# Kernel tuning notes

Hardware: AMD Instinct MI355X
Metric: run time of the kernel (lower is better)

The kernel has to match this reference:

```python
import jax, jax.numpy as jnp
import numpy as np

N_NODES = 200000
N_BONDS = 220000
D = 128


def setup_inputs() -> dict:
    key = jax.random.key(0)
    ks = jax.random.split(key, 8)
    h = jax.random.normal(ks[0], (N_NODES, D), dtype=jnp.float32)
    src = jax.random.randint(ks[1], (N_BONDS,), 0, N_NODES, dtype=jnp.int64)
    dst = jax.random.randint(ks[2], (N_BONDS,), 0, N_NODES, dtype=jnp.int64)
    # MLP params (Sequential: Linear(256,128)+ReLU, Linear(128,128)+ReLU, Linear(128,2))
    W1 = jax.random.normal(ks[3], (2 * D, 128), dtype=jnp.float32) * (1.0 / np.sqrt(2 * D))
    b1 = jnp.zeros((128,), dtype=jnp.float32)
    W2 = jax.random.normal(ks[4], (128, 128), dtype=jnp.float32) * (1.0 / np.sqrt(128))
    b2 = jnp.zeros((128,), dtype=jnp.float32)
    W3 = jax.random.normal(ks[5], (128, 2), dtype=jnp.float32) * (1.0 / np.sqrt(128))
    b3 = jnp.zeros((2,), dtype=jnp.float32)
    return {"h": h, "src": src, "dst": dst,
            "W1": W1, "b1": b1, "W2": W2, "b2": b2, "W3": W3, "b3": b3}


def _mlp(x, W1, b1, W2, b2, W3, b3):
    x = jax.nn.relu(x @ W1 + b1)
    x = jax.nn.relu(x @ W2 + b2)
    return x @ W3 + b3


def reference(h, src, dst, W1, b1, W2, b2, W3, b3):
    # forward edges: (src -> dst); reverse edges: (dst -> src)
    h_src = h[src]            # [E, D] gather
    h_dst = h[dst]            # [E, D] gather
    h_forward = jnp.concatenate([h_src, h_dst], axis=1)  # [E, 2D]
    h_reverse = jnp.concatenate([h_dst, h_src], axis=1)  # [E, 2D]
    return (_mlp(h_forward, W1, b1, W2, b2, W3, b3)
            + _mlp(h_reverse, W1, b1, W2, b2, W3, b3))
```

## Files before the change

kernel.cpp:

```cpp
#include <hip/hip_runtime.h>
#include <hip/hip_bf16.h>
#include <stdint.h>


typedef __attribute__((ext_vector_type(8))) short bf16x8;
typedef __attribute__((ext_vector_type(4))) float f32x4;

__device__ __forceinline__ float bf2f(unsigned u16) {
    union { unsigned u; float f; } v; v.u = u16 << 16;
    return v.f;
}
__device__ __forceinline__ unsigned short f2bf(float f) {
    union { float f; unsigned u; } v; v.f = f;
    unsigned u = v.u;
    unsigned r = u + 0x7FFFu + ((u >> 16) & 1u);
    return (unsigned short)(r >> 16);
}

__device__ __forceinline__ int swz(int f, int c) {
    return f * 128 + ((c ^ (f & 7)) << 3);
}

__device__ __forceinline__ bf16x8 cvt8(const float* p) {
    float4 x = *(const float4*)p;
    float4 y = *(const float4*)(p + 4);
    union { bf16x8 v; __hip_bfloat162 h[4]; } R;
    R.h[0] = __float22bfloat162_rn(float2{x.x, x.y});
    R.h[1] = __float22bfloat162_rn(float2{x.z, x.w});
    R.h[2] = __float22bfloat162_rn(float2{y.x, y.y});
    R.h[3] = __float22bfloat162_rn(float2{y.z, y.w});
    return R.v;
}

__device__ __forceinline__ bf16x8 addrelu8(uint4 a, uint4 b) {
    union { uint4 v; unsigned u[4]; } A, B;
    A.v = a; B.v = b;
    union { bf16x8 v; __hip_bfloat162 h[4]; } R;
#pragma unroll
    for (int i = 0; i < 4; ++i) {
        float a0 = bf2f(A.u[i] & 0xFFFFu), a1 = bf2f(A.u[i] >> 16);
        float b0 = bf2f(B.u[i] & 0xFFFFu), b1 = bf2f(B.u[i] >> 16);
        R.h[i] = __float22bfloat162_rn(float2{fmaxf(a0 + b0, 0.f),
                                              fmaxf(a1 + b1, 0.f)});
    }
    return R.v;
}

#define MFMA(a, b, c) __builtin_amdgcn_mfma_f32_16x16x32_bf16((a), (b), (c), 0, 0, 0)

__global__ void prep_weights(const float* __restrict__ W1,
                             const float* __restrict__ W2,
                             unsigned short* __restrict__ W1t,
                             unsigned short* __restrict__ W2t) {
    int idx = blockIdx.x * 256 + threadIdx.x;
    if (idx < 256 * 128) {
        int j = idx >> 7, k = idx & 127;
        float v = (j < 128) ? W1[k * 128 + j] : W1[(k + 128) * 128 + (j - 128)];
        W1t[idx] = f2bf(v);
    } else {
        int i2 = idx - 256 * 128;
        if (i2 < 128 * 128) {
            int n = i2 >> 7, k = i2 & 127;
            W2t[i2] = f2bf(W2[k * 128 + n]);
        }
    }
}

__global__ __launch_bounds__(512, 2) void node_proj(
    const float* __restrict__ h, const unsigned short* __restrict__ W1t,
    const float* __restrict__ b1, unsigned short* __restrict__ P, int nodes) {
    __shared__ unsigned short W1s[256 * 128];

    int t = threadIdx.x;
    int lane = t & 63;
    int wv = t >> 6;
    int ml = lane & 15, quad = lane >> 4;

    {
        int r = t >> 1, half = t & 1;
        const uint4* src = (const uint4*)(W1t + (size_t)r * 128 + half * 64);
#pragma unroll
        for (int i = 0; i < 8; ++i)
            *(uint4*)(W1s + swz(r, half * 8 + i)) = src[i];
    }

    int node = blockIdx.x * 128 + wv * 16 + ml;
    int nodeL = (node < nodes) ? node : (nodes - 1);
    const float* hrow = h + (size_t)nodeL * 128;
    bf16x8 bfrag[4];
#pragma unroll
    for (int kk = 0; kk < 4; ++kk)
        bfrag[kk] = cvt8(hrow + kk * 32 + quad * 8);

    __syncthreads();

    f32x4 acc[16] = {};
#pragma unroll
    for (int kk = 0; kk < 4; ++kk) {
#pragma unroll
        for (int ct = 0; ct < 16; ++ct) {
            bf16x8 afrag = *(const bf16x8*)(W1s + swz(ct * 16 + ml, kk * 4 + quad));
            acc[ct] = MFMA(afrag, bfrag[kk], acc[ct]);
        }
    }

    if (node < nodes) {
        unsigned short* prow = P + (size_t)node * 256;
#pragma unroll
        for (int ct = 0; ct < 16; ++ct) {
            int fbase = ct * 16 + quad * 4;
            float v0 = acc[ct][0], v1 = acc[ct][1];
            float v2 = acc[ct][2], v3 = acc[ct][3];
            if (fbase >= 128) {
                float4 bv = *(const float4*)(b1 + (fbase - 128));
                v0 += bv.x; v1 += bv.y; v2 += bv.z; v3 += bv.w;
            }
            union { uint2 u; __hip_bfloat162 h2[2]; } o;
            o.h2[0] = __float22bfloat162_rn(float2{v0, v1});
            o.h2[1] = __float22bfloat162_rn(float2{v2, v3});
            *(uint2*)(prow + fbase) = o.u;
        }
    }
}

__global__ __launch_bounds__(512, 2) void edge_mlp(
    const unsigned short* __restrict__ P, const int* __restrict__ src,
    const int* __restrict__ dst, const unsigned short* __restrict__ W2t,
    const float* __restrict__ b2, const float* __restrict__ W3,
    const float* __restrict__ b3, float* __restrict__ out, int E) {
    __shared__ unsigned short W2s[128 * 128];

    int t = threadIdx.x;
    int lane = t & 63;
    int wv = t >> 6;
    int ml = lane & 15, quad = lane >> 4;

    {
        int f = t >> 2, q4 = t & 3;
        const uint4* s = (const uint4*)(W2t + (size_t)f * 128 + q4 * 32);
#pragma unroll
        for (int i = 0; i < 4; ++i)
            *(uint4*)(W2s + swz(f, q4 * 4 + i)) = s[i];
    }

    int e = blockIdx.x * 128 + wv * 16 + ml;
    int ec = (e < E) ? e : (E - 1);
    int si = src[ec], di = dst[ec];
    const unsigned short* Ps = P + (size_t)si * 256;
    const unsigned short* Pd = P + (size_t)di * 256;

    uint4 g[4][4];
#pragma unroll
    for (int kk = 0; kk < 4; ++kk) {
        int ko = kk * 32 + quad * 8;
        g[kk][0] = *(const uint4*)(Ps + ko);
        g[kk][1] = *(const uint4*)(Ps + 128 + ko);
        g[kk][2] = *(const uint4*)(Pd + ko);
        g[kk][3] = *(const uint4*)(Pd + 128 + ko);
    }

    __syncthreads();

    f32x4 acc[2][8] = {};
#pragma unroll
    for (int kk = 0; kk < 4; ++kk) {
        bf16x8 afw = addrelu8(g[kk][0], g[kk][3]);
        bf16x8 arv = addrelu8(g[kk][2], g[kk][1]);
#pragma unroll
        for (int ct = 0; ct < 8; ++ct) {
            bf16x8 bfrag = *(const bf16x8*)(W2s + swz(ct * 16 + ml, kk * 4 + quad));
            acc[0][ct] = MFMA(afw, bfrag, acc[0][ct]);
            acc[1][ct] = MFMA(arv, bfrag, acc[1][ct]);
        }
    }

    float w30[8], w31[8], b2v[8];
#pragma unroll
    for (int ct = 0; ct < 8; ++ct) {
        int c = ct * 16 + ml;
        w30[ct] = W3[c * 2 + 0];
        w31[ct] = W3[c * 2 + 1];
        b2v[ct] = b2[c];
    }
    float p0[2][4], p1[2][4];
#pragma unroll
    for (int rt = 0; rt < 2; ++rt)
#pragma unroll
        for (int reg = 0; reg < 4; ++reg) { p0[rt][reg] = 0.f; p1[rt][reg] = 0.f; }
#pragma unroll
    for (int rt = 0; rt < 2; ++rt)
#pragma unroll
        for (int ct = 0; ct < 8; ++ct)
#pragma unroll
            for (int reg = 0; reg < 4; ++reg) {
                float h2 = fmaxf(acc[rt][ct][reg] + b2v[ct], 0.f);
                p0[rt][reg] += h2 * w30[ct];
                p1[rt][reg] += h2 * w31[ct];
            }
#pragma unroll
    for (int m = 1; m < 16; m <<= 1) {
#pragma unroll
        for (int rt = 0; rt < 2; ++rt)
#pragma unroll
            for (int reg = 0; reg < 4; ++reg) {
                p0[rt][reg] += __shfl_xor(p0[rt][reg], m);
                p1[rt][reg] += __shfl_xor(p1[rt][reg], m);
            }
    }

    if (ml < 2) {
        float bb = 2.f * b3[ml];
#pragma unroll
        for (int reg = 0; reg < 4; ++reg) {
            int ee = blockIdx.x * 128 + wv * 16 + quad * 4 + reg;
            if (ee < E) {
                float v = (ml == 0) ? (p0[0][reg] + p0[1][reg])
                                    : (p1[0][reg] + p1[1][reg]);
                out[(size_t)ee * 2 + ml] = v + bb;
            }
        }
    }
}

extern "C" void kernel_launch(void* const* d_in, const int* in_sizes, int n_in,
                              void* d_out, int out_size, void* d_ws, size_t ws_size,
                              hipStream_t stream) {
    (void)n_in; (void)out_size; (void)ws_size;
    const float* h  = (const float*)d_in[0];
    const int*   sr = (const int*)d_in[1];
    const int*   ds = (const int*)d_in[2];
    const float* W1 = (const float*)d_in[3];
    const float* b1 = (const float*)d_in[4];
    const float* W2 = (const float*)d_in[5];
    const float* b2 = (const float*)d_in[6];
    const float* W3 = (const float*)d_in[7];
    const float* b3 = (const float*)d_in[8];
    float* out = (float*)d_out;

    int nodes = in_sizes[0] / 128;
    int E = in_sizes[1];

    unsigned short* W1t = (unsigned short*)d_ws;
    unsigned short* W2t = W1t + 256 * 128;
    unsigned short* P   = W2t + 128 * 128;

    prep_weights<<<(256 * 128 + 128 * 128 + 255) / 256, 256, 0, stream>>>(W1, W2, W1t, W2t);

    int ntiles = (nodes + 127) / 128;
    node_proj<<<ntiles, 512, 0, stream>>>(h, W1t, b1, P, nodes);

    int etiles = (E + 127) / 128;
    edge_mlp<<<etiles, 512, 0, stream>>>(P, sr, ds, W2t, b2, W3, b3, out, E);
}
```

Measured before the change: 245.8 us.

## Make node_proj and edge_mlp persistent with software-prefetched next-tile loads

Both kernels become grid-stride persistent loops (node_proj capped at 512 blocks, edge_mlp at 256). The weight matrix is staged into LDS once per block instead of once per tile. While the current tile runs its MFMAs, the next tile's h rows or gathered P rows are loaded into registers, and the edge kernel also fetches edge indices two tiles ahead. This targets repeated weight-staging cost and exposed gather latency, at the price of extra register pressure and fewer resident blocks for latency hiding.

```diff
diff --git a/kernel.cpp b/kernel.cpp
--- a/kernel.cpp
+++ b/kernel.cpp
@@ -21,9 +21,7 @@
     return f * 128 + ((c ^ (f & 7)) << 3);
 }
 
-__device__ __forceinline__ bf16x8 cvt8(const float* p) {
-    float4 x = *(const float4*)p;
-    float4 y = *(const float4*)(p + 4);
+__device__ __forceinline__ bf16x8 cvt8r(float4 x, float4 y) {
     union { bf16x8 v; __hip_bfloat162 h[4]; } R;
     R.h[0] = __float22bfloat162_rn(float2{x.x, x.y});
     R.h[1] = __float22bfloat162_rn(float2{x.z, x.w});
@@ -68,7 +66,8 @@
 
 __global__ __launch_bounds__(512, 2) void node_proj(
     const float* __restrict__ h, const unsigned short* __restrict__ W1t,
-    const float* __restrict__ b1, unsigned short* __restrict__ P, int nodes) {
+    const float* __restrict__ b1, unsigned short* __restrict__ P,
+    int nodes, int ntiles) {
     __shared__ unsigned short W1s[256 * 128];
 
     int t = threadIdx.x;
@@ -84,41 +83,67 @@
             *(uint4*)(W1s + swz(r, half * 8 + i)) = src[i];
     }
 
-    int node = blockIdx.x * 128 + wv * 16 + ml;
-    int nodeL = (node < nodes) ? node : (nodes - 1);
-    const float* hrow = h + (size_t)nodeL * 128;
-    bf16x8 bfrag[4];
-#pragma unroll
-    for (int kk = 0; kk < 4; ++kk)
-        bfrag[kk] = cvt8(hrow + kk * 32 + quad * 8);
+    int tile = blockIdx.x;
+    float4 hreg[8];
+    if (tile < ntiles) {
+        int nd = tile * 128 + wv * 16 + ml;
+        if (nd >= nodes) nd = nodes - 1;
+        const float4* hp = (const float4*)(h + (size_t)nd * 128);
+#pragma unroll
+        for (int kk = 0; kk < 4; ++kk) {
+            hreg[2 * kk]     = hp[kk * 8 + quad * 2];
+            hreg[2 * kk + 1] = hp[kk * 8 + quad * 2 + 1];
+        }
+    }
 
     __syncthreads();
 
-    f32x4 acc[16] = {};
-#pragma unroll
-    for (int kk = 0; kk < 4; ++kk) {
-#pragma unroll
-        for (int ct = 0; ct < 16; ++ct) {
-            bf16x8 afrag = *(const bf16x8*)(W1s + swz(ct * 16 + ml, kk * 4 + quad));
-            acc[ct] = MFMA(afrag, bfrag[kk], acc[ct]);
-        }
-    }
-
-    if (node < nodes) {
-        unsigned short* prow = P + (size_t)node * 256;
-#pragma unroll
-        for (int ct = 0; ct < 16; ++ct) {
-            int fbase = ct * 16 + quad * 4;
-            float v0 = acc[ct][0], v1 = acc[ct][1];
-            float v2 = acc[ct][2], v3 = acc[ct][3];
-            if (fbase >= 128) {
-                float4 bv = *(const float4*)(b1 + (fbase - 128));
-                v0 += bv.x; v1 += bv.y; v2 += bv.z; v3 += bv.w;
-            }
-            union { uint2 u; __hip_bfloat162 h2[2]; } o;
-            o.h2[0] = __float22bfloat162_rn(float2{v0, v1});
-            o.h2[1] = __float22bfloat162_rn(float2{v2, v3});
-            *(uint2*)(prow + fbase) = o.u;
+    for (; tile < ntiles; tile += gridDim.x) {
+        bf16x8 bfrag[4];
+#pragma unroll
+        for (int kk = 0; kk < 4; ++kk)
+            bfrag[kk] = cvt8r(hreg[2 * kk], hreg[2 * kk + 1]);
+
+        int node = tile * 128 + wv * 16 + ml;
+
+        int ntile = tile + gridDim.x;
+        if (ntile < ntiles) {
+            int nd = ntile * 128 + wv * 16 + ml;
+            if (nd >= nodes) nd = nodes - 1;
+            const float4* hp = (const float4*)(h + (size_t)nd * 128);
+#pragma unroll
+            for (int kk = 0; kk < 4; ++kk) {
+                hreg[2 * kk]     = hp[kk * 8 + quad * 2];
+                hreg[2 * kk + 1] = hp[kk * 8 + quad * 2 + 1];
+            }
+        }
+
+        f32x4 acc[16] = {};
+#pragma unroll
+        for (int kk = 0; kk < 4; ++kk) {
+#pragma unroll
+            for (int ct = 0; ct < 16; ++ct) {
+                bf16x8 afrag = *(const bf16x8*)(W1s + swz(ct * 16 + ml, kk * 4 + quad));
+                acc[ct] = MFMA(afrag, bfrag[kk], acc[ct]);
+            }
+        }
+
+        if (node < nodes) {
+            unsigned short* prow = P + (size_t)node * 256;
+#pragma unroll
+            for (int ct = 0; ct < 16; ++ct) {
+                int fbase = ct * 16 + quad * 4;
+                float v0 = acc[ct][0], v1 = acc[ct][1];
+                float v2 = acc[ct][2], v3 = acc[ct][3];
+                if (fbase >= 128) {
+                    float4 bv = *(const float4*)(b1 + (fbase - 128));
+                    v0 += bv.x; v1 += bv.y; v2 += bv.z; v3 += bv.w;
+                }
+                union { uint2 u; __hip_bfloat162 h2[2]; } o;
+                o.h2[0] = __float22bfloat162_rn(float2{v0, v1});
+                o.h2[1] = __float22bfloat162_rn(float2{v2, v3});
+                *(uint2*)(prow + fbase) = o.u;
+            }
         }
     }
 }
@@ -127,7 +152,7 @@
     const unsigned short* __restrict__ P, const int* __restrict__ src,
     const int* __restrict__ dst, const unsigned short* __restrict__ W2t,
     const float* __restrict__ b2, const float* __restrict__ W3,
-    const float* __restrict__ b3, float* __restrict__ out, int E) {
+    const float* __restrict__ b3, float* __restrict__ out, int E, int etiles) {
     __shared__ unsigned short W2s[128 * 128];
 
     int t = threadIdx.x;
@@ -141,37 +166,6 @@
 #pragma unroll
         for (int i = 0; i < 4; ++i)
             *(uint4*)(W2s + swz(f, q4 * 4 + i)) = s[i];
-    }
-
-    int e = blockIdx.x * 128 + wv * 16 + ml;
-    int ec = (e < E) ? e : (E - 1);
-    int si = src[ec], di = dst[ec];
-    const unsigned short* Ps = P + (size_t)si * 256;
-    const unsigned short* Pd = P + (size_t)di * 256;
-
-    uint4 g[4][4];
-#pragma unroll
-    for (int kk = 0; kk < 4; ++kk) {
-        int ko = kk * 32 + quad * 8;
-        g[kk][0] = *(const uint4*)(Ps + ko);
-        g[kk][1] = *(const uint4*)(Ps + 128 + ko);
-        g[kk][2] = *(const uint4*)(Pd + ko);
-        g[kk][3] = *(const uint4*)(Pd + 128 + ko);
-    }
-
-    __syncthreads();
-
-    f32x4 acc[2][8] = {};
-#pragma unroll
-    for (int kk = 0; kk < 4; ++kk) {
-        bf16x8 afw = addrelu8(g[kk][0], g[kk][3]);
-        bf16x8 arv = addrelu8(g[kk][2], g[kk][1]);
-#pragma unroll
-        for (int ct = 0; ct < 8; ++ct) {
-            bf16x8 bfrag = *(const bf16x8*)(W2s + swz(ct * 16 + ml, kk * 4 + quad));
-            acc[0][ct] = MFMA(afw, bfrag, acc[0][ct]);
-            acc[1][ct] = MFMA(arv, bfrag, acc[1][ct]);
-        }
     }
 
     float w30[8], w31[8], b2v[8];
@@ -182,41 +176,112 @@
         w31[ct] = W3[c * 2 + 1];
         b2v[ct] = b2[c];
     }
-    float p0[2][4], p1[2][4];
-#pragma unroll
-    for (int rt = 0; rt < 2; ++rt)
-#pragma unroll
-        for (int reg = 0; reg < 4; ++reg) { p0[rt][reg] = 0.f; p1[rt][reg] = 0.f; }
-#pragma unroll
-    for (int rt = 0; rt < 2; ++rt)
-#pragma unroll
-        for (int ct = 0; ct < 8; ++ct)
+    float bb0 = 2.f * b3[0], bb1 = 2.f * b3[1];
+
+    int tile = blockIdx.x;
+
+    int si = 0, di = 0, si2 = 0, di2 = 0;
+    uint4 g[4][4];
+    if (tile < etiles) {
+        int e0 = tile * 128 + wv * 16 + ml;
+        int ec = (e0 < E) ? e0 : (E - 1);
+        si = src[ec]; di = dst[ec];
+        const unsigned short* Ps = P + (size_t)si * 256;
+        const unsigned short* Pd = P + (size_t)di * 256;
+#pragma unroll
+        for (int kk = 0; kk < 4; ++kk) {
+            int ko = kk * 32 + quad * 8;
+            g[kk][0] = *(const uint4*)(Ps + ko);
+            g[kk][1] = *(const uint4*)(Ps + 128 + ko);
+            g[kk][2] = *(const uint4*)(Pd + ko);
+            g[kk][3] = *(const uint4*)(Pd + 128 + ko);
+        }
+        int t2 = tile + gridDim.x;
+        if (t2 < etiles) {
+            int e2 = t2 * 128 + wv * 16 + ml;
+            int ec2 = (e2 < E) ? e2 : (E - 1);
+            si2 = src[ec2]; di2 = dst[ec2];
+        }
+    }
+
+    __syncthreads();
+
+    for (; tile < etiles; tile += gridDim.x) {
+        bf16x8 afw[4], arv[4];
+#pragma unroll
+        for (int kk = 0; kk < 4; ++kk) {
+            afw[kk] = addrelu8(g[kk][0], g[kk][3]);
+            arv[kk] = addrelu8(g[kk][2], g[kk][1]);
+        }
+
+        int ebase = tile * 128 + wv * 16;
+
+        int ntile = tile + gridDim.x;
+        if (ntile < etiles) {
+            const unsigned short* Ps = P + (size_t)si2 * 256;
+            const unsigned short* Pd = P + (size_t)di2 * 256;
+#pragma unroll
+            for (int kk = 0; kk < 4; ++kk) {
+                int ko = kk * 32 + quad * 8;
+                g[kk][0] = *(const uint4*)(Ps + ko);
+                g[kk][1] = *(const uint4*)(Ps + 128 + ko);
+                g[kk][2] = *(const uint4*)(Pd + ko);
+                g[kk][3] = *(const uint4*)(Pd + 128 + ko);
+            }
+            int t2 = ntile + gridDim.x;
+            if (t2 < etiles) {
+                int e2 = t2 * 128 + wv * 16 + ml;
+                int ec2 = (e2 < E) ? e2 : (E - 1);
+                si2 = src[ec2]; di2 = dst[ec2];
+            }
+        }
+
+        f32x4 acc[2][8] = {};
+#pragma unroll
+        for (int kk = 0; kk < 4; ++kk) {
+#pragma unroll
+            for (int ct = 0; ct < 8; ++ct) {
+                bf16x8 bfrag = *(const bf16x8*)(W2s + swz(ct * 16 + ml, kk * 4 + quad));
+                acc[0][ct] = MFMA(afw[kk], bfrag, acc[0][ct]);
+                acc[1][ct] = MFMA(arv[kk], bfrag, acc[1][ct]);
+            }
+        }
+
+        float p0[2][4], p1[2][4];
+#pragma unroll
+        for (int rt = 0; rt < 2; ++rt)
+#pragma unroll
+            for (int reg = 0; reg < 4; ++reg) { p0[rt][reg] = 0.f; p1[rt][reg] = 0.f; }
+#pragma unroll
+        for (int rt = 0; rt < 2; ++rt)
+#pragma unroll
+            for (int ct = 0; ct < 8; ++ct)
+#pragma unroll
+                for (int reg = 0; reg < 4; ++reg) {
+                    float h2 = fmaxf(acc[rt][ct][reg] + b2v[ct], 0.f);
+                    p0[rt][reg] += h2 * w30[ct];
+                    p1[rt][reg] += h2 * w31[ct];
+                }
+#pragma unroll
+        for (int m = 1; m < 16; m <<= 1) {
+#pragma unroll
+            for (int rt = 0; rt < 2; ++rt)
+#pragma unroll
+                for (int reg = 0; reg < 4; ++reg) {
+                    p0[rt][reg] += __shfl_xor(p0[rt][reg], m);
+                    p1[rt][reg] += __shfl_xor(p1[rt][reg], m);
+                }
+        }
+
+        if (ml < 2) {
 #pragma unroll
             for (int reg = 0; reg < 4; ++reg) {
-                float h2 = fmaxf(acc[rt][ct][reg] + b2v[ct], 0.f);
-                p0[rt][reg] += h2 * w30[ct];
-                p1[rt][reg] += h2 * w31[ct];
-            }
-#pragma unroll
-    for (int m = 1; m < 16; m <<= 1) {
-#pragma unroll
-        for (int rt = 0; rt < 2; ++rt)
-#pragma unroll
-            for (int reg = 0; reg < 4; ++reg) {
-                p0[rt][reg] += __shfl_xor(p0[rt][reg], m);
-                p1[rt][reg] += __shfl_xor(p1[rt][reg], m);
-            }
-    }
-
-    if (ml < 2) {
-        float bb = 2.f * b3[ml];
-#pragma unroll
-        for (int reg = 0; reg < 4; ++reg) {
-            int ee = blockIdx.x * 128 + wv * 16 + quad * 4 + reg;
-            if (ee < E) {
-                float v = (ml == 0) ? (p0[0][reg] + p0[1][reg])
-                                    : (p1[0][reg] + p1[1][reg]);
-                out[(size_t)ee * 2 + ml] = v + bb;
+                int ee = ebase + quad * 4 + reg;
+                if (ee < E) {
+                    float v = (ml == 0) ? (p0[0][reg] + p0[1][reg] + bb0)
+                                        : (p1[0][reg] + p1[1][reg] + bb1);
+                    out[(size_t)ee * 2 + ml] = v;
+                }
             }
         }
     }
@@ -247,8 +312,10 @@
     prep_weights<<<(256 * 128 + 128 * 128 + 255) / 256, 256, 0, stream>>>(W1, W2, W1t, W2t);
 
     int ntiles = (nodes + 127) / 128;
-    node_proj<<<ntiles, 512, 0, stream>>>(h, W1t, b1, P, nodes);
+    int ngrid = (ntiles < 512) ? ntiles : 512;
+    node_proj<<<ngrid, 512, 0, stream>>>(h, W1t, b1, P, nodes, ntiles);
 
     int etiles = (E + 127) / 128;
-    edge_mlp<<<etiles, 512, 0, stream>>>(P, sr, ds, W2t, b2, W3, b3, out, E);
-}
+    int egrid = (etiles < 256) ? etiles : 256;
+    edge_mlp<<<egrid, 512, 0, stream>>>(P, sr, ds, W2t, b2, W3, b3, out, E, etiles);
+}
```

Measured after the change: 427.0 us. 1.74x slower.

## Fold weight prep into kernels and stage node projection stores through LDS

Applied to the files above, without the earlier changes.

Removes the separate prep_weights launch. node_proj and edge_mlp now read the fp32 weights directly, transpose them, convert them to bf16 and write them into LDS, which drops one kernel launch and the workspace round trip. node_proj also stages its bf16 output through a swizzled LDS slice so each node row is written to global memory with coalesced 16-byte stores rather than scattered 8-byte stores. The trade-off is that every block now does strided fp32 weight loads and conversion work, and an extra barrier is added.

```diff
diff --git a/kernel.cpp b/kernel.cpp
--- a/kernel.cpp
+++ b/kernel.cpp
@@ -10,26 +10,9 @@
     union { unsigned u; float f; } v; v.u = u16 << 16;
     return v.f;
 }
-__device__ __forceinline__ unsigned short f2bf(float f) {
-    union { float f; unsigned u; } v; v.f = f;
-    unsigned u = v.u;
-    unsigned r = u + 0x7FFFu + ((u >> 16) & 1u);
-    return (unsigned short)(r >> 16);
-}
 
 __device__ __forceinline__ int swz(int f, int c) {
     return f * 128 + ((c ^ (f & 7)) << 3);
-}
-
-__device__ __forceinline__ bf16x8 cvt8(const float* p) {
-    float4 x = *(const float4*)p;
-    float4 y = *(const float4*)(p + 4);
-    union { bf16x8 v; __hip_bfloat162 h[4]; } R;
-    R.h[0] = __float22bfloat162_rn(float2{x.x, x.y});
-    R.h[1] = __float22bfloat162_rn(float2{x.z, x.w});
-    R.h[2] = __float22bfloat162_rn(float2{y.x, y.y});
-    R.h[3] = __float22bfloat162_rn(float2{y.z, y.w});
-    return R.v;
 }
 
 __device__ __forceinline__ bf16x8 addrelu8(uint4 a, uint4 b) {
@@ -46,28 +29,18 @@
     return R.v;
 }
 
+__device__ __forceinline__ uint4 pack8(const float* v) {
+    union { uint4 u; __hip_bfloat162 h[4]; } R;
+#pragma unroll
+    for (int i = 0; i < 4; ++i)
+        R.h[i] = __float22bfloat162_rn(float2{v[2 * i], v[2 * i + 1]});
+    return R.u;
+}
+
 #define MFMA(a, b, c) __builtin_amdgcn_mfma_f32_16x16x32_bf16((a), (b), (c), 0, 0, 0)
 
-__global__ void prep_weights(const float* __restrict__ W1,
-                             const float* __restrict__ W2,
-                             unsigned short* __restrict__ W1t,
-                             unsigned short* __restrict__ W2t) {
-    int idx = blockIdx.x * 256 + threadIdx.x;
-    if (idx < 256 * 128) {
-        int j = idx >> 7, k = idx & 127;
-        float v = (j < 128) ? W1[k * 128 + j] : W1[(k + 128) * 128 + (j - 128)];
-        W1t[idx] = f2bf(v);
-    } else {
-        int i2 = idx - 256 * 128;
-        if (i2 < 128 * 128) {
-            int n = i2 >> 7, k = i2 & 127;
-            W2t[i2] = f2bf(W2[k * 128 + n]);
-        }
-    }
-}
-
 __global__ __launch_bounds__(512, 2) void node_proj(
-    const float* __restrict__ h, const unsigned short* __restrict__ W1t,
+    const float* __restrict__ h, const float* __restrict__ W1,
     const float* __restrict__ b1, unsigned short* __restrict__ P, int nodes) {
     __shared__ unsigned short W1s[256 * 128];
 
@@ -77,22 +50,43 @@
     int ml = lane & 15, quad = lane >> 4;
 
     {
-        int r = t >> 1, half = t & 1;
-        const uint4* src = (const uint4*)(W1t + (size_t)r * 128 + half * 64);
-#pragma unroll
-        for (int i = 0; i < 8; ++i)
-            *(uint4*)(W1s + swz(r, half * 8 + i)) = src[i];
-    }
-
-    int node = blockIdx.x * 128 + wv * 16 + ml;
+        int j = t >> 1, half = t & 1;
+        const float* col = (j < 128) ? (W1 + j) : (W1 + 128 * 128 + (j - 128));
+#pragma unroll
+        for (int ci = 0; ci < 8; ++ci) {
+            int c = half * 8 + ci;
+            float v[8];
+#pragma unroll
+            for (int l = 0; l < 8; ++l)
+                v[l] = col[(c * 8 + l) * 128];
+            *(uint4*)(W1s + swz(j, c)) = pack8(v);
+        }
+    }
+
+    int tile = blockIdx.x;
+    int node = tile * 128 + wv * 16 + ml;
     int nodeL = (node < nodes) ? node : (nodes - 1);
-    const float* hrow = h + (size_t)nodeL * 128;
+    const float4* hp = (const float4*)(h + (size_t)nodeL * 128);
+    float4 hreg[8];
+#pragma unroll
+    for (int kk = 0; kk < 4; ++kk) {
+        hreg[2 * kk]     = hp[kk * 8 + quad * 2];
+        hreg[2 * kk + 1] = hp[kk * 8 + quad * 2 + 1];
+    }
+
+    __syncthreads();
+
     bf16x8 bfrag[4];
 #pragma unroll
-    for (int kk = 0; kk < 4; ++kk)
-        bfrag[kk] = cvt8(hrow + kk * 32 + quad * 8);
-
-    __syncthreads();
+    for (int kk = 0; kk < 4; ++kk) {
+        union { bf16x8 v; __hip_bfloat162 hh[4]; } R;
+        float4 x = hreg[2 * kk], y = hreg[2 * kk + 1];
+        R.hh[0] = __float22bfloat162_rn(float2{x.x, x.y});
+        R.hh[1] = __float22bfloat162_rn(float2{x.z, x.w});
+        R.hh[2] = __float22bfloat162_rn(float2{y.x, y.y});
+        R.hh[3] = __float22bfloat162_rn(float2{y.z, y.w});
+        bfrag[kk] = R.v;
+    }
 
     f32x4 acc[16] = {};
 #pragma unroll
@@ -104,28 +98,39 @@
         }
     }
 
-    if (node < nodes) {
-        unsigned short* prow = P + (size_t)node * 256;
-#pragma unroll
-        for (int ct = 0; ct < 16; ++ct) {
-            int fbase = ct * 16 + quad * 4;
-            float v0 = acc[ct][0], v1 = acc[ct][1];
-            float v2 = acc[ct][2], v3 = acc[ct][3];
-            if (fbase >= 128) {
-                float4 bv = *(const float4*)(b1 + (fbase - 128));
-                v0 += bv.x; v1 += bv.y; v2 += bv.z; v3 += bv.w;
-            }
-            union { uint2 u; __hip_bfloat162 h2[2]; } o;
-            o.h2[0] = __float22bfloat162_rn(float2{v0, v1});
-            o.h2[1] = __float22bfloat162_rn(float2{v2, v3});
-            *(uint2*)(prow + fbase) = o.u;
-        }
+    __syncthreads();
+
+    unsigned* slice = (unsigned*)W1s + wv * 2048;
+#pragma unroll
+    for (int ct = 0; ct < 16; ++ct) {
+        int fbase = ct * 16 + quad * 4;
+        float v0 = acc[ct][0], v1 = acc[ct][1];
+        float v2 = acc[ct][2], v3 = acc[ct][3];
+        if (fbase >= 128) {
+            float4 bv = *(const float4*)(b1 + (fbase - 128));
+            v0 += bv.x; v1 += bv.y; v2 += bv.z; v3 += bv.w;
+        }
+        union { uint2 u; __hip_bfloat162 h2[2]; } o;
+        o.h2[0] = __float22bfloat162_rn(float2{v0, v1});
+        o.h2[1] = __float22bfloat162_rn(float2{v2, v3});
+        int c = ct * 2 + (quad >> 1);
+        int idx = ml * 128 + ((c ^ ml) << 2) + ((quad & 1) << 1);
+        *(uint2*)(slice + idx) = o.u;
+    }
+#pragma unroll
+    for (int i = 0; i < 8; ++i) {
+        int n = i * 2 + (lane >> 5);
+        int cr = lane & 31;
+        uint4 val = *(const uint4*)(slice + n * 128 + ((cr ^ n) << 2));
+        int gnode = tile * 128 + wv * 16 + n;
+        if (gnode < nodes)
+            *(uint4*)((unsigned*)(P + (size_t)gnode * 256) + cr * 4) = val;
     }
 }
 
 __global__ __launch_bounds__(512, 2) void edge_mlp(
     const unsigned short* __restrict__ P, const int* __restrict__ src,
-    const int* __restrict__ dst, const unsigned short* __restrict__ W2t,
+    const int* __restrict__ dst, const float* __restrict__ W2,
     const float* __restrict__ b2, const float* __restrict__ W3,
     const float* __restrict__ b3, float* __restrict__ out, int E) {
     __shared__ unsigned short W2s[128 * 128];
@@ -137,10 +142,16 @@
 
     {
         int f = t >> 2, q4 = t & 3;
-        const uint4* s = (const uint4*)(W2t + (size_t)f * 128 + q4 * 32);
-#pragma unroll
-        for (int i = 0; i < 4; ++i)
-            *(uint4*)(W2s + swz(f, q4 * 4 + i)) = s[i];
+        const float* col = W2 + f;
+#pragma unroll
+        for (int ci = 0; ci < 4; ++ci) {
+            int c = q4 * 4 + ci;
+            float v[8];
+#pragma unroll
+            for (int l = 0; l < 8; ++l)
+                v[l] = col[(c * 8 + l) * 128];
+            *(uint4*)(W2s + swz(f, c)) = pack8(v);
+        }
     }
 
     int e = blockIdx.x * 128 + wv * 16 + ml;
@@ -240,15 +251,11 @@
     int nodes = in_sizes[0] / 128;
     int E = in_sizes[1];
 
-    unsigned short* W1t = (unsigned short*)d_ws;
-    unsigned short* W2t = W1t + 256 * 128;
-    unsigned short* P   = W2t + 128 * 128;
-
-    prep_weights<<<(256 * 128 + 128 * 128 + 255) / 256, 256, 0, stream>>>(W1, W2, W1t, W2t);
+    unsigned short* P = (unsigned short*)d_ws;
 
     int ntiles = (nodes + 127) / 128;
-    node_proj<<<ntiles, 512, 0, stream>>>(h, W1t, b1, P, nodes);
+    node_proj<<<ntiles, 512, 0, stream>>>(h, W1, b1, P, nodes);
 
     int etiles = (E + 127) / 128;
-    edge_mlp<<<etiles, 512, 0, stream>>>(P, sr, ds, W2t, b2, W3, b3, out, E);
-}
+    edge_mlp<<<etiles, 512, 0, stream>>>(P, sr, ds, W2, b2, W3, b3, out, E);
+}
```

Measured after the change: 247.1 us. No clear change (+0.6%).
